# Optimization experiments

Measured on AMD Instinct MI355X. Metric: run time of the kernel, lower is better.

## Reference

```python
import jax, jax.numpy as jnp
import numpy as np
from jax import lax

S, V, DW = 2048, 50000, 400     # seq_len, word vocab, word emb dim
CV, DC = 8, 32                  # casing vocab / dim
PV, DP = 50, 64                 # POS vocab / dim
H, C = 768, 13                  # lstm hidden (per direction), num tag classes
DIN = DW + DC + DP              # 496 lstm input dim


def setup_inputs() -> dict:
    key = jax.random.key(0)
    ks = jax.random.split(key, 18)
    r = lambda k, sh, s=0.02: (jax.random.normal(k, sh) * s).astype(jnp.float32)
    return {
        "x": jax.random.randint(ks[0], (S,), 0, V),
        "casing": jax.random.randint(ks[1], (S,), 0, CV),
        "pos": jax.random.randint(ks[2], (S,), 0, PV),
        "word_emb": r(ks[3], (V, DW)),
        "casing_emb": r(ks[4], (CV, DC)),
        "pos_emb": r(ks[5], (PV, DP)),
        "Wih_f": r(ks[6], (4 * H, DIN)),
        "Whh_f": r(ks[7], (4 * H, H)),
        "b_f": jnp.zeros((4 * H,), jnp.float32),
        "Wih_b": r(ks[8], (4 * H, DIN)),
        "Whh_b": r(ks[9], (4 * H, H)),
        "b_b": jnp.zeros((4 * H,), jnp.float32),
        "Wc": r(ks[10], (C, 2 * H)),
        "bc": jnp.zeros((C,), jnp.float32),
        "start_trans": r(ks[11], (C,), 0.1),
        "end_trans": r(ks[12], (C,), 0.1),
        "trans": r(ks[13], (C, C), 0.1),
        "h0": jnp.zeros((2, H), jnp.float32),
        "c0": jnp.zeros((2, H), jnp.float32),
    }


def _lstm(xg, Whh, h0, c0):
    # xg: (S, 4H) precomputed input-to-hidden gates; PyTorch gate order i,f,g,o
    def step(carry, g_in):
        h, c = carry
        g = g_in + h @ Whh.T
        i, f, gg, o = jnp.split(g, 4)
        c = jax.nn.sigmoid(f) * c + jax.nn.sigmoid(i) * jnp.tanh(gg)
        h = jax.nn.sigmoid(o) * jnp.tanh(c)
        return (h, c), h
    _, hs = lax.scan(step, (h0, c0), xg)
    return hs  # (S, H)


def reference(x, casing, pos, word_emb, casing_emb, pos_emb,
              Wih_f, Whh_f, b_f, Wih_b, Whh_b, b_b, Wc, bc,
              start_trans, end_trans, trans, h0, c0):
    # embedding concat -> (S, DIN)
    emb = jnp.concatenate([word_emb[x], casing_emb[casing], pos_emb[pos]], axis=-1)
    # weight-dropped LSTM (eval mode: DropConnect identity), bidirectional
    hs_f = _lstm(emb @ Wih_f.T + b_f, Whh_f, h0[0], c0[0])
    hs_b = _lstm((emb @ Wih_b.T + b_b)[::-1], Whh_b, h0[1], c0[1])[::-1]
    o = jnp.concatenate([hs_f, hs_b], axis=-1) @ Wc.T + bc  # (S, C)
    tag_scores = jax.nn.log_softmax(o, axis=1)
    # CRF Viterbi decode (torchcrf-style), batch of 1 (the unsqueeze(0))
    score0 = start_trans + tag_scores[0]
    def vstep(score, em):
        cand = score[:, None] + trans            # (prev C, next C)
        bp = jnp.argmax(cand, axis=0)
        return jnp.max(cand, axis=0) + em, bp
    score, bps = lax.scan(vstep, score0, tag_scores[1:])
    last = jnp.argmax(score + end_trans)
    def back(tag, bp):
        prev = bp[tag]
        return prev, prev
    _, prevs = lax.scan(back, last, bps[::-1])
    tags = jnp.concatenate([prevs[::-1], last[None]])  # (S,) best path
    return tag_scores, tags
```

## Files before the change

### kernel.cpp

```cpp
#include <hip/hip_runtime.h>
#include <hip/hip_bf16.h>


#define SEQ  2048
#define DINW 496
#define HDIM 768
#define G4   3072
#define CDIM 13
#define NWG  48
#define JPW  16
#define HINT_SPIN (1u << 16)
#define DATA_SPIN (1u << 14)
#define DEADBIT 0x40000000u

__device__ __forceinline__ float sigf(float x) { return 1.0f / (1.0f + __expf(-x)); }
__device__ __forceinline__ float tanhf_fast(float x) {
    float ax = fabsf(x);
    float e  = __expf(-2.0f * ax);
    float t  = (1.0f - e) / (1.0f + e);
    return copysignf(t, x);
}

__global__ __launch_bounds__(256) void k_gemm_xg(
    const int* __restrict__ x, const int* __restrict__ casing, const int* __restrict__ pos,
    const float* __restrict__ we, const float* __restrict__ ce, const float* __restrict__ pe,
    const float* __restrict__ Wih_f, const float* __restrict__ b_f,
    const float* __restrict__ Wih_b, const float* __restrict__ b_b,
    __hip_bfloat16* __restrict__ xg_f, __hip_bfloat16* __restrict__ xg_b)
{
    __shared__ float As[16][68];
    __shared__ float Bs[16][68];
    int dir = blockIdx.z;
    const float* B    = dir ? Wih_b : Wih_f;
    const float* bias = dir ? b_b   : b_f;
    __hip_bfloat16* C = dir ? xg_b  : xg_f;
    int n0 = blockIdx.x * 64, m0 = blockIdx.y * 64;
    int tid = threadIdx.x;
    int tx = tid & 15, ty = tid >> 4;
    int lr = tid >> 2, lk = (tid & 3) * 4;

    int m = m0 + lr;
    const float* arow_w = we + (size_t)x[m] * 400;
    const float* arow_c = ce + (size_t)casing[m] * 32;
    const float* arow_p = pe + (size_t)pos[m] * 64;

    float acc[4][4] = {};
    for (int k0 = 0; k0 < DINW; k0 += 16) {
        int c0 = k0 + lk;
        float4 a;
        if (c0 < 400)      a = *(const float4*)(arow_w + c0);
        else if (c0 < 432) a = *(const float4*)(arow_c + (c0 - 400));
        else               a = *(const float4*)(arow_p + (c0 - 432));
        float4 b = *(const float4*)(B + (size_t)(n0 + lr) * DINW + c0);
        __syncthreads();
        As[lk + 0][lr] = a.x; As[lk + 1][lr] = a.y; As[lk + 2][lr] = a.z; As[lk + 3][lr] = a.w;
        Bs[lk + 0][lr] = b.x; Bs[lk + 1][lr] = b.y; Bs[lk + 2][lr] = b.z; Bs[lk + 3][lr] = b.w;
        __syncthreads();
        #pragma unroll
        for (int k = 0; k < 16; k++) {
            float4 av = *(const float4*)&As[k][ty * 4];
            float4 bv = *(const float4*)&Bs[k][tx * 4];
            float aa[4] = {av.x, av.y, av.z, av.w};
            float bb[4] = {bv.x, bv.y, bv.z, bv.w};
            #pragma unroll
            for (int i = 0; i < 4; i++)
                #pragma unroll
                for (int jj = 0; jj < 4; jj++)
                    acc[i][jj] += aa[i] * bb[jj];
        }
    }
    float4 bs4 = *(const float4*)(bias + n0 + tx * 4);
    float bb4[4] = {bs4.x, bs4.y, bs4.z, bs4.w};
    #pragma unroll
    for (int i = 0; i < 4; i++) {
        union { __hip_bfloat16 h[4]; ushort4 u; } cv;
        #pragma unroll
        for (int jj = 0; jj < 4; jj++)
            cv.h[jj] = __float2bfloat16(acc[i][jj] + bb4[jj]);
        *(ushort4*)(C + (size_t)(m0 + ty * 4 + i) * G4 + n0 + tx * 4) = cv.u;
    }
}

__global__ __launch_bounds__(1024) void k_lstm(
    const __hip_bfloat16* __restrict__ xg_f, const __hip_bfloat16* __restrict__ xg_b,
    const float* __restrict__ Whh_f, const float* __restrict__ Whh_b,
    const float* __restrict__ h0, const float* __restrict__ c0v,
    float* __restrict__ hs_f, float* __restrict__ hs_b,
    unsigned long long* __restrict__ msg, unsigned* __restrict__ done,
    unsigned* __restrict__ abortw)
{
    __shared__ float hbuf[2][HDIM];
    __shared__ unsigned lflag;

    int wg = blockIdx.x;
    int dir = wg & 1, slot = wg >> 1;
    const __hip_bfloat16* xg = dir ? xg_b : xg_f;
    const float* Whh = dir ? Whh_b : Whh_f;
    float* hs        = dir ? hs_b  : hs_f;
    unsigned long long* mdir = msg + (size_t)dir * 2 * HDIM;
    unsigned* ddir = done + dir * 64;

    int tid = threadIdx.x, lane = tid & 63, wv = tid >> 6;
    int q = lane >> 4, gl = lane & 15;
    int j = slot * JPW + wv;

    float w[48];
    const float* wr = Whh + (size_t)(q * HDIM + j) * HDIM;
    #pragma unroll
    for (int m = 0; m < 12; m++) {
        float4 f4 = *(const float4*)(wr + gl * 4 + m * 64);
        w[m * 4 + 0] = f4.x; w[m * 4 + 1] = f4.y;
        w[m * 4 + 2] = f4.z; w[m * 4 + 3] = f4.w;
    }
    float cst = c0v[dir * HDIM + j];

    if (tid == 0) lflag = 0;
    __syncthreads();

    for (int t = 0; t < SEQ; t++) {
        int xrow = dir ? (SEQ - 1 - t) : t;
        const __hip_bfloat16* xga = xg + (size_t)xrow * G4 + j;
        float xv0 = __bfloat162float(xga[0]);
        float xv1 = __bfloat162float(xga[HDIM]);
        float xv2 = __bfloat162float(xga[2 * HDIM]);
        float xv3 = __bfloat162float(xga[3 * HDIM]);

        int par = (t & 1) ^ 1;

        if (wv == 0) {
            bool dead = false;
            if (t == 0) {
                #pragma unroll
                for (int m = 0; m < 12; m++)
                    hbuf[1][m * 64 + lane] = h0[dir * HDIM + m * 64 + lane];
            } else {
                int bidx = (lane < NWG) ? lane : 0;
                unsigned iter = 0;
                bool hok;
                do {
                    unsigned v = __hip_atomic_load(&ddir[bidx],
                                    __ATOMIC_RELAXED, __HIP_MEMORY_SCOPE_AGENT);
                    unsigned ab = __hip_atomic_load(abortw,
                                    __ATOMIC_RELAXED, __HIP_MEMORY_SCOPE_AGENT);
                    if (ab) { dead = true; break; }
                    hok = __all((lane < NWG) ? (v >= (unsigned)t) : true);
                } while (!hok && ++iter < HINT_SPIN);
                if (!dead && !hok) dead = true;
                if (!dead) {
                    const unsigned long long* g = mdir + (size_t)par * HDIM;
                    unsigned long long vals[12];
                    unsigned iter2 = 0;
                    bool ok;
                    do {
                        ok = true;
                        #pragma unroll
                        for (int m = 0; m < 12; m++)
                            vals[m] = __hip_atomic_load(&g[m * 64 + lane],
                                                        __ATOMIC_RELAXED, __HIP_MEMORY_SCOPE_AGENT);
                        #pragma unroll
                        for (int m = 0; m < 12; m++)
                            ok &= ((unsigned)(vals[m] >> 32) == (unsigned)t);
                        ok = __all(ok);
                    } while (!ok && ++iter2 < DATA_SPIN);
                    if (!ok) dead = true;
                    #pragma unroll
                    for (int m = 0; m < 12; m++) {
                        union { unsigned u; float f; } cvt;
                        cvt.u = (unsigned)vals[m];
                        hbuf[par][m * 64 + lane] = cvt.f;
                    }
                }
                if (dead && lane == 0) {
                    __hip_atomic_store(abortw, 1u,
                                       __ATOMIC_RELAXED, __HIP_MEMORY_SCOPE_AGENT);
                    __hip_atomic_store(&ddir[slot], 0x7FFFFFFFu,
                                       __ATOMIC_RELAXED, __HIP_MEMORY_SCOPE_AGENT);
                }
            }
            __threadfence_block();
            if (lane == 0)
                __hip_atomic_store(&lflag, (unsigned)(t + 1) | (dead ? DEADBIT : 0u),
                                   __ATOMIC_RELAXED, __HIP_MEMORY_SCOPE_WORKGROUP);
        }

        unsigned f;
        do {
            f = __hip_atomic_load(&lflag, __ATOMIC_RELAXED, __HIP_MEMORY_SCOPE_WORKGROUP);
        } while ((f & ~DEADBIT) < (unsigned)(t + 1));
        if (f & DEADBIT) break;

        float acc = 0.f;
        #pragma unroll
        for (int m = 0; m < 12; m++) {
            float4 f4 = *(const float4*)&hbuf[par][gl * 4 + m * 64];
            acc += w[m * 4 + 0] * f4.x + w[m * 4 + 1] * f4.y
                 + w[m * 4 + 2] * f4.z + w[m * 4 + 3] * f4.w;
        }
        acc += __shfl_xor(acc, 1);
        acc += __shfl_xor(acc, 2);
        acc += __shfl_xor(acc, 4);
        acc += __shfl_xor(acc, 8);
        float si = __shfl(acc, 0),  sf = __shfl(acc, 16);
        float sg = __shfl(acc, 32), so = __shfl(acc, 48);

        float gi = sigf(xv0 + si), gf = sigf(xv1 + sf);
        float gg = tanhf_fast(xv2 + sg), go = sigf(xv3 + so);
        cst = gf * cst + gi * gg;
        float h = go * tanhf_fast(cst);

        if (lane == 0) {
            int hrow = dir ? (SEQ - 1 - t) : t;
            hs[(size_t)hrow * HDIM + j] = h;
            union { float f; unsigned u; } cvt; cvt.f = h;
            unsigned long long word = ((unsigned long long)(unsigned)(t + 1) << 32)
                                    | (unsigned long long)cvt.u;
            __hip_atomic_store(&mdir[(size_t)(t & 1) * HDIM + j], word,
                               __ATOMIC_RELAXED, __HIP_MEMORY_SCOPE_AGENT);
            if (wv == 0)
                __hip_atomic_store(&ddir[slot], (unsigned)(t + 1),
                                   __ATOMIC_RELAXED, __HIP_MEMORY_SCOPE_AGENT);
        }
    }
}

__global__ __launch_bounds__(256) void k_head(
    const float* __restrict__ hs_f, const float* __restrict__ hs_b,
    const float* __restrict__ Wc, const float* __restrict__ bc,
    float* __restrict__ out)
{
    int tid = threadIdx.x, lane = tid & 63, wv = tid >> 6;
    int row = blockIdx.x * 4 + wv;
    const float* src = (lane < 32) ? (hs_f + (size_t)row * HDIM + lane * 24)
                                   : (hs_b + (size_t)row * HDIM + (lane - 32) * 24);
    float hvv[24];
    #pragma unroll
    for (int k = 0; k < 6; k++) {
        float4 f4 = *(const float4*)(src + k * 4);
        hvv[k * 4 + 0] = f4.x; hvv[k * 4 + 1] = f4.y;
        hvv[k * 4 + 2] = f4.z; hvv[k * 4 + 3] = f4.w;
    }
    int off = (lane < 32) ? lane * 24 : 768 + (lane - 32) * 24;
    float o[13];
    #pragma unroll
    for (int n = 0; n < CDIM; n++) {
        const float* wr2 = Wc + (size_t)n * 1536 + off;
        float s0 = 0.f, s1 = 0.f, s2 = 0.f, s3 = 0.f;
        #pragma unroll
        for (int k = 0; k < 6; k++) {
            float4 w4 = *(const float4*)(wr2 + k * 4);
            s0 += w4.x * hvv[k * 4 + 0];
            s1 += w4.y * hvv[k * 4 + 1];
            s2 += w4.z * hvv[k * 4 + 2];
            s3 += w4.w * hvv[k * 4 + 3];
        }
        o[n] = (s0 + s1) + (s2 + s3);
    }
    #pragma unroll
    for (int n = 0; n < CDIM; n++) {
        #pragma unroll
        for (int d = 1; d < 64; d <<= 1) o[n] += __shfl_xor(o[n], d);
        o[n] += bc[n];
    }
    float m = o[0];
    #pragma unroll
    for (int n = 1; n < CDIM; n++) m = fmaxf(m, o[n]);
    float sum = 0.f;
    #pragma unroll
    for (int n = 0; n < CDIM; n++) sum += __expf(o[n] - m);
    float ls = m + __logf(sum);
    if (lane == 0) {
        #pragma unroll
        for (int n = 0; n < CDIM; n++) out[(size_t)row * CDIM + n] = o[n] - ls;
    }
}

__global__ __launch_bounds__(64) void k_viterbi(
    const float* __restrict__ ts, const float* __restrict__ st,
    const float* __restrict__ en, const float* __restrict__ tr,
    float* __restrict__ tags_out)
{
    __shared__ unsigned char bp[SEQ - 1][16];
    __shared__ unsigned char path[SEQ];
    int n = threadIdx.x;
    bool act = n < CDIM;
    float trn[CDIM];
    #pragma unroll
    for (int p = 0; p < CDIM; p++) trn[p] = act ? tr[p * CDIM + n] : -1e30f;
    float score = act ? (st[n] + ts[n]) : -1e30f;

    for (int s = 1; s < SEQ; s++) {
        float em = act ? ts[(size_t)s * CDIM + n] : 0.f;
        float sp[CDIM];
        #pragma unroll
        for (int p = 0; p < CDIM; p++) sp[p] = __shfl(score, p);
        float best = -1e30f; int arg = 0;
        #pragma unroll
        for (int p = 0; p < CDIM; p++) {
            float v = sp[p] + trn[p];
            if (v > best) { best = v; arg = p; }
        }
        score = best + em;
        if (act) bp[s - 1][n] = (unsigned char)arg;
    }
    float fin = act ? (score + en[n]) : -1e30f;
    float fv[CDIM];
    #pragma unroll
    for (int p = 0; p < CDIM; p++) fv[p] = __shfl(fin, p);
    __syncthreads();
    if (n == 0) {
        float best = -1e30f; int last = 0;
        #pragma unroll
        for (int p = 0; p < CDIM; p++) { if (fv[p] > best) { best = fv[p]; last = p; } }
        int cur = last;
        path[SEQ - 1] = (unsigned char)cur;
        for (int s = SEQ - 2; s >= 0; s--) { cur = bp[s][cur]; path[s] = (unsigned char)cur; }
    }
    __syncthreads();
    for (int i = n; i < SEQ; i += 64) tags_out[i] = (float)path[i];
}

__global__ void k_zero(float* p, int n) {
    int i = blockIdx.x * 256 + threadIdx.x;
    if (i < n) p[i] = 0.f;
}

extern "C" void kernel_launch(void* const* d_in, const int* in_sizes, int n_in,
                              void* d_out, int out_size, void* d_ws, size_t ws_size,
                              hipStream_t stream)
{
    const int*   x      = (const int*)d_in[0];
    const int*   casing = (const int*)d_in[1];
    const int*   pos    = (const int*)d_in[2];
    const float* we     = (const float*)d_in[3];
    const float* ce     = (const float*)d_in[4];
    const float* pe     = (const float*)d_in[5];
    const float* Wih_f  = (const float*)d_in[6];
    const float* Whh_f  = (const float*)d_in[7];
    const float* b_f    = (const float*)d_in[8];
    const float* Wih_b  = (const float*)d_in[9];
    const float* Whh_b  = (const float*)d_in[10];
    const float* b_b    = (const float*)d_in[11];
    const float* Wc     = (const float*)d_in[12];
    const float* bc     = (const float*)d_in[13];
    const float* strt   = (const float*)d_in[14];
    const float* endt   = (const float*)d_in[15];
    const float* trans  = (const float*)d_in[16];
    const float* h0     = (const float*)d_in[17];
    const float* c0     = (const float*)d_in[18];

    const size_t need = 37773828;
    if (ws_size < need) {
        k_zero<<<(out_size + 255) / 256, 256, 0, stream>>>((float*)d_out, out_size);
        return;
    }
    char* wsb = (char*)d_ws;
    float* hs_f = (float*)(wsb);
    float* hs_b = (float*)(wsb + 6291456);
    __hip_bfloat16* xg_f = (__hip_bfloat16*)(wsb + 12582912);
    __hip_bfloat16* xg_b = (__hip_bfloat16*)(wsb + 25165824);
    unsigned long long* msg = (unsigned long long*)(wsb + 37748736);
    unsigned* done = (unsigned*)(wsb + 37773312);
    unsigned* abortw = (unsigned*)(wsb + 37773824);

    hipMemsetAsync(msg, 0, 24576 + 512 + 4, stream);

    k_gemm_xg<<<dim3(G4 / 64, SEQ / 64, 2), 256, 0, stream>>>(
        x, casing, pos, we, ce, pe, Wih_f, b_f, Wih_b, b_b, xg_f, xg_b);
    k_lstm<<<2 * NWG, 1024, 0, stream>>>(
        xg_f, xg_b, Whh_f, Whh_b, h0, c0, hs_f, hs_b, msg, done, abortw);
    k_head<<<SEQ / 4, 256, 0, stream>>>(hs_f, hs_b, Wc, bc, (float*)d_out);
    k_viterbi<<<1, 64, 0, stream>>>(
        (const float*)d_out, strt, endt, trans, (float*)d_out + (size_t)SEQ * CDIM);
}
```

Baseline: 7.272 ms.

## Drop done-counter handshake and poll tagged h messages directly with partial refresh

Removes the per-workgroup done-counter array and its polling phase. Consumers now spin only on the sequence-tagged h words, reloading just the chunks that are still stale. The LDS flag handoff inside each workgroup is replaced by __syncthreads barriers, one before the matvec and one after the h publish. This takes one global polling round trip off the critical path of each recurrent step, at the cost of more global traffic while spinning and two full-block barriers per step.

```diff
diff --git a/kernel.cpp b/kernel.cpp
--- a/kernel.cpp
+++ b/kernel.cpp
@@ -9,9 +9,7 @@
 #define CDIM 13
 #define NWG  48
 #define JPW  16
-#define HINT_SPIN (1u << 16)
 #define DATA_SPIN (1u << 14)
-#define DEADBIT 0x40000000u
 
 __device__ __forceinline__ float sigf(float x) { return 1.0f / (1.0f + __expf(-x)); }
 __device__ __forceinline__ float tanhf_fast(float x) {
@@ -86,11 +84,10 @@
     const float* __restrict__ Whh_f, const float* __restrict__ Whh_b,
     const float* __restrict__ h0, const float* __restrict__ c0v,
     float* __restrict__ hs_f, float* __restrict__ hs_b,
-    unsigned long long* __restrict__ msg, unsigned* __restrict__ done,
-    unsigned* __restrict__ abortw)
+    unsigned long long* __restrict__ msg, unsigned* __restrict__ abortw)
 {
     __shared__ float hbuf[2][HDIM];
-    __shared__ unsigned lflag;
+    __shared__ unsigned sdead;
 
     int wg = blockIdx.x;
     int dir = wg & 1, slot = wg >> 1;
@@ -98,7 +95,6 @@
     const float* Whh = dir ? Whh_b : Whh_f;
     float* hs        = dir ? hs_b  : hs_f;
     unsigned long long* mdir = msg + (size_t)dir * 2 * HDIM;
-    unsigned* ddir = done + dir * 64;
 
     int tid = threadIdx.x, lane = tid & 63, wv = tid >> 6;
     int q = lane >> 4, gl = lane & 15;
@@ -114,8 +110,7 @@
     }
     float cst = c0v[dir * HDIM + j];
 
-    if (tid == 0) lflag = 0;
-    __syncthreads();
+    if (tid == 0) sdead = 0;
 
     for (int t = 0; t < SEQ; t++) {
         int xrow = dir ? (SEQ - 1 - t) : t;
@@ -128,66 +123,47 @@
         int par = (t & 1) ^ 1;
 
         if (wv == 0) {
-            bool dead = false;
             if (t == 0) {
                 #pragma unroll
                 for (int m = 0; m < 12; m++)
                     hbuf[1][m * 64 + lane] = h0[dir * HDIM + m * 64 + lane];
             } else {
-                int bidx = (lane < NWG) ? lane : 0;
-                unsigned iter = 0;
-                bool hok;
-                do {
-                    unsigned v = __hip_atomic_load(&ddir[bidx],
-                                    __ATOMIC_RELAXED, __HIP_MEMORY_SCOPE_AGENT);
+                const unsigned long long* g = mdir + (size_t)par * HDIM;
+                unsigned long long vals[12];
+                unsigned freshm = 0;
+                unsigned rounds = 0;
+                bool dead = false;
+                for (;;) {
+                    #pragma unroll
+                    for (int m = 0; m < 12; m++)
+                        if (!(freshm & (1u << m)))
+                            vals[m] = __hip_atomic_load(&g[m * 64 + lane],
+                                        __ATOMIC_RELAXED, __HIP_MEMORY_SCOPE_AGENT);
+                    #pragma unroll
+                    for (int m = 0; m < 12; m++)
+                        if ((unsigned)(vals[m] >> 32) == (unsigned)t)
+                            freshm |= (1u << m);
+                    if (__all(freshm == 0xFFFu)) break;
                     unsigned ab = __hip_atomic_load(abortw,
                                     __ATOMIC_RELAXED, __HIP_MEMORY_SCOPE_AGENT);
-                    if (ab) { dead = true; break; }
-                    hok = __all((lane < NWG) ? (v >= (unsigned)t) : true);
-                } while (!hok && ++iter < HINT_SPIN);
-                if (!dead && !hok) dead = true;
-                if (!dead) {
-                    const unsigned long long* g = mdir + (size_t)par * HDIM;
-                    unsigned long long vals[12];
-                    unsigned iter2 = 0;
-                    bool ok;
-                    do {
-                        ok = true;
-                        #pragma unroll
-                        for (int m = 0; m < 12; m++)
-                            vals[m] = __hip_atomic_load(&g[m * 64 + lane],
-                                                        __ATOMIC_RELAXED, __HIP_MEMORY_SCOPE_AGENT);
-                        #pragma unroll
-                        for (int m = 0; m < 12; m++)
-                            ok &= ((unsigned)(vals[m] >> 32) == (unsigned)t);
-                        ok = __all(ok);
-                    } while (!ok && ++iter2 < DATA_SPIN);
-                    if (!ok) dead = true;
-                    #pragma unroll
-                    for (int m = 0; m < 12; m++) {
-                        union { unsigned u; float f; } cvt;
-                        cvt.u = (unsigned)vals[m];
-                        hbuf[par][m * 64 + lane] = cvt.f;
-                    }
+                    if (ab || ++rounds >= DATA_SPIN) { dead = true; break; }
+                }
+                #pragma unroll
+                for (int m = 0; m < 12; m++) {
+                    union { unsigned u; float f; } cvt;
+                    cvt.u = (unsigned)vals[m];
+                    hbuf[par][m * 64 + lane] = cvt.f;
                 }
                 if (dead && lane == 0) {
                     __hip_atomic_store(abortw, 1u,
                                        __ATOMIC_RELAXED, __HIP_MEMORY_SCOPE_AGENT);
-                    __hip_atomic_store(&ddir[slot], 0x7FFFFFFFu,
-                                       __ATOMIC_RELAXED, __HIP_MEMORY_SCOPE_AGENT);
+                    sdead = 1;
                 }
             }
-            __threadfence_block();
-            if (lane == 0)
-                __hip_atomic_store(&lflag, (unsigned)(t + 1) | (dead ? DEADBIT : 0u),
-                                   __ATOMIC_RELAXED, __HIP_MEMORY_SCOPE_WORKGROUP);
-        }
-
-        unsigned f;
-        do {
-            f = __hip_atomic_load(&lflag, __ATOMIC_RELAXED, __HIP_MEMORY_SCOPE_WORKGROUP);
-        } while ((f & ~DEADBIT) < (unsigned)(t + 1));
-        if (f & DEADBIT) break;
+        }
+
+        __syncthreads();
+        if (sdead) break;
 
         float acc = 0.f;
         #pragma unroll
@@ -216,10 +192,8 @@
                                     | (unsigned long long)cvt.u;
             __hip_atomic_store(&mdir[(size_t)(t & 1) * HDIM + j], word,
                                __ATOMIC_RELAXED, __HIP_MEMORY_SCOPE_AGENT);
-            if (wv == 0)
-                __hip_atomic_store(&ddir[slot], (unsigned)(t + 1),
-                                   __ATOMIC_RELAXED, __HIP_MEMORY_SCOPE_AGENT);
-        }
+        }
+        __syncthreads();
     }
 }
 
@@ -348,7 +322,7 @@
     const float* h0     = (const float*)d_in[17];
     const float* c0     = (const float*)d_in[18];
 
-    const size_t need = 37773828;
+    const size_t need = 37773316;
     if (ws_size < need) {
         k_zero<<<(out_size + 255) / 256, 256, 0, stream>>>((float*)d_out, out_size);
         return;
@@ -359,15 +333,14 @@
     __hip_bfloat16* xg_f = (__hip_bfloat16*)(wsb + 12582912);
     __hip_bfloat16* xg_b = (__hip_bfloat16*)(wsb + 25165824);
     unsigned long long* msg = (unsigned long long*)(wsb + 37748736);
-    unsigned* done = (unsigned*)(wsb + 37773312);
-    unsigned* abortw = (unsigned*)(wsb + 37773824);
-
-    hipMemsetAsync(msg, 0, 24576 + 512 + 4, stream);
+    unsigned* abortw = (unsigned*)(wsb + 37773312);
+
+    hipMemsetAsync(msg, 0, 24576 + 4, stream);
 
     k_gemm_xg<<<dim3(G4 / 64, SEQ / 64, 2), 256, 0, stream>>>(
         x, casing, pos, we, ce, pe, Wih_f, b_f, Wih_b, b_b, xg_f, xg_b);
     k_lstm<<<2 * NWG, 1024, 0, stream>>>(
-        xg_f, xg_b, Whh_f, Whh_b, h0, c0, hs_f, hs_b, msg, done, abortw);
+        xg_f, xg_b, Whh_f, Whh_b, h0, c0, hs_f, hs_b, msg, abortw);
     k_head<<<SEQ / 4, 256, 0, stream>>>(hs_f, hs_b, Wc, bc, (float*)d_out);
     k_viterbi<<<1, 64, 0, stream>>>(
         (const float*)d_out, strt, endt, trans, (float*)d_out + (size_t)SEQ * CDIM);
```

After: 7.366 ms. About the same (+1.3%).
